# Performance work log

Hardware: AMD Instinct MI355X
Metric: run time of the kernel (lower is better)

Reference implementation:

```python
import jax, jax.numpy as jnp
import numpy as np

N_DATA = 542080   # N320 grid points
N_TRUNC = 40320   # O96 grid points
E_DOWN = 1084160
E_UP = 1084160
FEAT = 64


def setup_inputs() -> dict:
    key = jax.random.key(0)
    ks = jax.random.split(key, 7)
    x = jax.random.normal(ks[0], (2, 2, 1, N_DATA, FEAT), dtype=jnp.float32)
    down_src = jax.random.randint(ks[1], (E_DOWN,), 0, N_DATA)
    down_dst = jax.random.randint(ks[2], (E_DOWN,), 0, N_TRUNC)
    down_w = jax.random.uniform(ks[3], (E_DOWN,), dtype=jnp.float32)
    up_src = jax.random.randint(ks[4], (E_UP,), 0, N_TRUNC)
    up_dst = jax.random.randint(ks[5], (E_UP,), 0, N_DATA)
    up_w = jax.random.uniform(ks[6], (E_UP,), dtype=jnp.float32)
    return {"x": x, "down_src": down_src, "down_dst": down_dst, "down_w": down_w,
            "up_src": up_src, "up_dst": up_dst, "up_w": up_w}


def _sparse_project(h, src, dst, w, n_out):
    """Edge-weighted sparse projection: out[d] = sum_{e: dst[e]=d} w[e] * h[src[e]].

    h: (BE, n_in, F) -> (BE, n_out, F). Equivalent to left-multiplying by the
    sparse matrix A[dst, src] = w (summing duplicates), as SparseProjector does.
    """
    msgs = h[:, src, :] * w[None, :, None]            # (BE, E, F) gather + weight
    msgs = jnp.swapaxes(msgs, 0, 1)                   # (E, BE, F)
    out = jax.ops.segment_sum(msgs, dst, num_segments=n_out)  # (n_out, BE, F)
    return jnp.swapaxes(out, 0, 1)                    # (BE, n_out, F)


def reference(x, down_src, down_dst, down_w, up_src, up_dst, up_w):
    B, T, Ens, N, F = x.shape
    h = x[:, -1, ...]                                 # take last time step: (B, Ens, N, F)
    h = h.reshape(B * Ens, N, F)                      # (batch ensemble) grid features
    h = _sparse_project(h, down_src, down_dst, down_w, N_TRUNC)  # coarse grid
    h = _sparse_project(h, up_src, up_dst, up_w, N)              # back to full grid
    return h.reshape(B, Ens, N, F)
```

## Files before the change

### kernel.cpp

```cpp
#include <hip/hip_runtime.h>

#define FEAT 64
#define N_DATA 542080
#define N_TRUNC 40320
#define SCAN_TILE 4096


__global__ void histogram_dst(const int* __restrict__ dst, int n_edges,
                              int* __restrict__ counts) {
    int e = blockIdx.x * blockDim.x + threadIdx.x;
    if (e < n_edges) atomicAdd(&counts[dst[e]], 1);
}

__global__ void scan_block_sums(const int* __restrict__ counts, int n,
                                int* __restrict__ blockSums) {
    __shared__ int lds[256];
    int tid = threadIdx.x;
    int base = blockIdx.x * SCAN_TILE + tid * 16;
    int s = 0;
    #pragma unroll
    for (int i = 0; i < 16; ++i) {
        int idx = base + i;
        s += (idx < n) ? counts[idx] : 0;
    }
    lds[tid] = s;
    __syncthreads();
    for (int off = 128; off > 0; off >>= 1) {
        if (tid < off) lds[tid] += lds[tid + off];
        __syncthreads();
    }
    if (tid == 0) blockSums[blockIdx.x] = lds[0];
}

__global__ void scan_exclusive_blocksums(int* __restrict__ blockSums, int nblocks) {
    if (blockIdx.x == 0 && threadIdx.x == 0) {
        int acc = 0;
        for (int i = 0; i < nblocks; ++i) {
            int v = blockSums[i];
            blockSums[i] = acc;
            acc += v;
        }
    }
}

__global__ void scan_write_offsets(const int* __restrict__ counts, int n,
                                   const int* __restrict__ blockSums,
                                   int* __restrict__ offsets, int total_edges) {
    __shared__ int lds[256];
    int tid = threadIdx.x;
    int base = blockIdx.x * SCAN_TILE + tid * 16;
    int local[16];
    int s = 0;
    #pragma unroll
    for (int i = 0; i < 16; ++i) {
        int idx = base + i;
        int v = (idx < n) ? counts[idx] : 0;
        local[i] = s;
        s += v;
    }
    lds[tid] = s;
    __syncthreads();
    for (int off = 1; off < 256; off <<= 1) {
        int v = (tid >= off) ? lds[tid - off] : 0;
        __syncthreads();
        if (tid >= off) lds[tid] += v;
        __syncthreads();
    }
    int threadOffset = (tid == 0) ? 0 : lds[tid - 1];
    int blockOffset = blockSums[blockIdx.x];
    #pragma unroll
    for (int i = 0; i < 16; ++i) {
        int idx = base + i;
        if (idx < n) offsets[idx] = blockOffset + threadOffset + local[i];
    }
    if (blockIdx.x == 0 && tid == 0) offsets[n] = total_edges;
}

__global__ void build_csr(const int* __restrict__ src, const int* __restrict__ dst,
                          const float* __restrict__ w, int n_edges,
                          const int* __restrict__ offsets, int* __restrict__ cursor,
                          int2* __restrict__ csr_pair) {
    int e = blockIdx.x * blockDim.x + threadIdx.x;
    if (e >= n_edges) return;
    int d = dst[e];
    int pos = offsets[d] + atomicAdd(&cursor[d], 1);
    int2 p;
    p.x = src[e];
    p.y = __float_as_int(w[e]);
    csr_pair[pos] = p;
}

__global__ __launch_bounds__(256) void sparse_gather(
    const float* __restrict__ h, size_t h_bstride,
    float* __restrict__ out, size_t out_bstride,
    const int* __restrict__ offsets,
    const int2* __restrict__ csr_pair,
    int n_out)
{
    int id = blockIdx.x * blockDim.x + threadIdx.x;
    int d = id >> 4;
    int c = (id & 15) * 4;
    if (d >= n_out) return;

    int beg = offsets[d];
    int end = offsets[d + 1];

    float4 acc0 = make_float4(0.f, 0.f, 0.f, 0.f);
    float4 acc1 = make_float4(0.f, 0.f, 0.f, 0.f);

    for (int p = beg; p < end; ++p) {
        int2 pr = csr_pair[p];
        int   s  = pr.x;
        float ww = __int_as_float(pr.y);
        const float* row0 = h + (size_t)s * FEAT + c;
        const float* row1 = row0 + h_bstride;
        float4 v0 = *reinterpret_cast<const float4*>(row0);
        float4 v1 = *reinterpret_cast<const float4*>(row1);
        acc0.x += ww * v0.x; acc0.y += ww * v0.y;
        acc0.z += ww * v0.z; acc0.w += ww * v0.w;
        acc1.x += ww * v1.x; acc1.y += ww * v1.y;
        acc1.z += ww * v1.z; acc1.w += ww * v1.w;
    }
    float* o0 = out + (size_t)d * FEAT + c;
    *reinterpret_cast<float4*>(o0) = acc0;
    *reinterpret_cast<float4*>(o0 + out_bstride) = acc1;
}

__global__ __launch_bounds__(256) void sparse_project_atomic(
    const float* __restrict__ h, size_t h_bstride,
    float* __restrict__ out, size_t out_bstride,
    const int* __restrict__ src, const int* __restrict__ dst,
    const float* __restrict__ w, int n_edges)
{
    int id = blockIdx.x * blockDim.x + threadIdx.x;
    int e = id >> 4;
    int c = (id & 15) * 4;
    if (e >= n_edges) return;
    int b = blockIdx.y;
    const float* hb = h + (size_t)b * h_bstride;
    float*       ob = out + (size_t)b * out_bstride;
    int   s  = src[e];
    int   d  = dst[e];
    float ww = w[e];
    const float4 v = *reinterpret_cast<const float4*>(hb + (size_t)s * FEAT + c);
    float* op = ob + (size_t)d * FEAT + c;
    atomicAdd(op + 0, ww * v.x);
    atomicAdd(op + 1, ww * v.y);
    atomicAdd(op + 2, ww * v.z);
    atomicAdd(op + 3, ww * v.w);
}

static inline size_t align16(size_t v) { return (v + 15) & ~(size_t)15; }

extern "C" void kernel_launch(void* const* d_in, const int* in_sizes, int n_in,
                              void* d_out, int out_size, void* d_ws, size_t ws_size,
                              hipStream_t stream) {
    const float* x        = (const float*)d_in[0];
    const int*   down_src = (const int*)d_in[1];
    const int*   down_dst = (const int*)d_in[2];
    const float* down_w   = (const float*)d_in[3];
    const int*   up_src   = (const int*)d_in[4];
    const int*   up_dst   = (const int*)d_in[5];
    const float* up_w     = (const float*)d_in[6];
    float* out = (float*)d_out;

    const int e_down = in_sizes[1];
    const int e_up   = in_sizes[4];

    const float* x_last = x + (size_t)N_DATA * FEAT;
    const size_t x_bstride = (size_t)2 * N_DATA * FEAT;

    char* ws = (char*)d_ws;
    size_t off = 0;
    float* h_trunc   = (float*)(ws + off); off += align16((size_t)2 * N_TRUNC * FEAT * 4);
    int*   up_off    = (int*)(ws + off);   off += align16(((size_t)N_DATA + 1) * 4);
    int*   down_off  = (int*)(ws + off);   off += align16(((size_t)N_TRUNC + 1) * 4);
    int*   up_cur    = (int*)(ws + off);   off += align16((size_t)N_DATA * 4);
    int*   down_cur  = (int*)(ws + off);   off += align16((size_t)N_TRUNC * 4);
    int2*  up_csr    = (int2*)(ws + off);  off += align16((size_t)e_up * 8);
    int2*  down_csr  = (int2*)(ws + off);  off += align16((size_t)e_down * 8);
    int*   blockSums = (int*)(ws + off);   off += align16(1024);
    const size_t needed = off;

    if (ws_size < needed) {
        hipMemsetAsync(h_trunc, 0, (size_t)2 * N_TRUNC * FEAT * 4, stream);
        hipMemsetAsync(out, 0, (size_t)out_size * sizeof(float), stream);
        dim3 g1((e_down * 16 + 255) / 256, 2);
        sparse_project_atomic<<<g1, 256, 0, stream>>>(
            x_last, x_bstride, h_trunc, (size_t)N_TRUNC * FEAT,
            down_src, down_dst, down_w, e_down);
        dim3 g2((e_up * 16 + 255) / 256, 2);
        sparse_project_atomic<<<g2, 256, 0, stream>>>(
            h_trunc, (size_t)N_TRUNC * FEAT, out, (size_t)N_DATA * FEAT,
            up_src, up_dst, up_w, e_up);
        return;
    }

    const int nblk_down = (N_TRUNC + SCAN_TILE - 1) / SCAN_TILE;
    const int nblk_up   = (N_DATA  + SCAN_TILE - 1) / SCAN_TILE;

    hipMemsetAsync(down_cur, 0, (size_t)N_TRUNC * 4, stream);
    histogram_dst<<<(e_down + 255) / 256, 256, 0, stream>>>(down_dst, e_down, down_cur);
    scan_block_sums<<<nblk_down, 256, 0, stream>>>(down_cur, N_TRUNC, blockSums);
    scan_exclusive_blocksums<<<1, 64, 0, stream>>>(blockSums, nblk_down);
    scan_write_offsets<<<nblk_down, 256, 0, stream>>>(down_cur, N_TRUNC, blockSums, down_off, e_down);
    hipMemsetAsync(down_cur, 0, (size_t)N_TRUNC * 4, stream);
    build_csr<<<(e_down + 255) / 256, 256, 0, stream>>>(
        down_src, down_dst, down_w, e_down, down_off, down_cur, down_csr);

    hipMemsetAsync(up_cur, 0, (size_t)N_DATA * 4, stream);
    histogram_dst<<<(e_up + 255) / 256, 256, 0, stream>>>(up_dst, e_up, up_cur);
    scan_block_sums<<<nblk_up, 256, 0, stream>>>(up_cur, N_DATA, blockSums);
    scan_exclusive_blocksums<<<1, 64, 0, stream>>>(blockSums, nblk_up);
    scan_write_offsets<<<nblk_up, 256, 0, stream>>>(up_cur, N_DATA, blockSums, up_off, e_up);
    hipMemsetAsync(up_cur, 0, (size_t)N_DATA * 4, stream);
    build_csr<<<(e_up + 255) / 256, 256, 0, stream>>>(
        up_src, up_dst, up_w, e_up, up_off, up_cur, up_csr);

    {
        int threads = N_TRUNC * 16;
        sparse_gather<<<(threads + 255) / 256, 256, 0, stream>>>(
            x_last, x_bstride,
            h_trunc, (size_t)N_TRUNC * FEAT,
            down_off, down_csr, N_TRUNC);
    }
    {
        int threads = N_DATA * 16;
        sparse_gather<<<(threads + 255) / 256, 256, 0, stream>>>(
            h_trunc, (size_t)N_TRUNC * FEAT,
            out, (size_t)N_DATA * FEAT,
            up_off, up_csr, N_DATA);
    }
}
```

Baseline: 1.120 ms.

## Merge down/up CSR builds into one pass, unroll gather, use nontemporal output stores

The two CSR construction pipelines are merged into a single combined bucket space (down then up destinations), cutting the number of launches and memsets roughly in half. The serial block-sum scan is replaced with a parallel LDS scan, and count reset moves into the offset-writing kernel. The gather loop is unrolled by two to keep more loads in flight, and the final output uses nontemporal stores. The combined offsets rely on the up-pass offsets already including e_down, which matches the shared csr_all indexing.

```diff
diff --git a/kernel.cpp b/kernel.cpp
--- a/kernel.cpp
+++ b/kernel.cpp
@@ -3,13 +3,21 @@
 #define FEAT 64
 #define N_DATA 542080
 #define N_TRUNC 40320
+#define NB_TOTAL (N_TRUNC + N_DATA)
 #define SCAN_TILE 4096
 
-
-__global__ void histogram_dst(const int* __restrict__ dst, int n_edges,
-                              int* __restrict__ counts) {
+typedef float nfloat4 __attribute__((ext_vector_type(4)));
+
+
+__global__ void histogram_both(const int* __restrict__ ddst, int e_down,
+                               const int* __restrict__ udst, int e_up,
+                               int* __restrict__ counts) {
     int e = blockIdx.x * blockDim.x + threadIdx.x;
-    if (e < n_edges) atomicAdd(&counts[dst[e]], 1);
+    if (e < e_down) {
+        atomicAdd(&counts[ddst[e]], 1);
+    } else if (e < e_down + e_up) {
+        atomicAdd(&counts[N_TRUNC + udst[e - e_down]], 1);
+    }
 }
 
 __global__ void scan_block_sums(const int* __restrict__ counts, int n,
@@ -32,18 +40,21 @@
     if (tid == 0) blockSums[blockIdx.x] = lds[0];
 }
 
-__global__ void scan_exclusive_blocksums(int* __restrict__ blockSums, int nblocks) {
-    if (blockIdx.x == 0 && threadIdx.x == 0) {
-        int acc = 0;
-        for (int i = 0; i < nblocks; ++i) {
-            int v = blockSums[i];
-            blockSums[i] = acc;
-            acc += v;
-        }
-    }
-}
-
-__global__ void scan_write_offsets(const int* __restrict__ counts, int n,
+__global__ void scan_sums_block(int* __restrict__ blockSums, int nblocks) {
+    __shared__ int lds[256];
+    int tid = threadIdx.x;
+    lds[tid] = (tid < nblocks) ? blockSums[tid] : 0;
+    __syncthreads();
+    for (int off = 1; off < 256; off <<= 1) {
+        int v = (tid >= off) ? lds[tid - off] : 0;
+        __syncthreads();
+        if (tid >= off) lds[tid] += v;
+        __syncthreads();
+    }
+    if (tid < nblocks) blockSums[tid] = (tid == 0) ? 0 : lds[tid - 1];
+}
+
+__global__ void scan_write_offsets(int* __restrict__ counts, int n,
                                    const int* __restrict__ blockSums,
                                    int* __restrict__ offsets, int total_edges) {
     __shared__ int lds[256];
@@ -71,25 +82,38 @@
     #pragma unroll
     for (int i = 0; i < 16; ++i) {
         int idx = base + i;
-        if (idx < n) offsets[idx] = blockOffset + threadOffset + local[i];
+        if (idx < n) {
+            offsets[idx] = blockOffset + threadOffset + local[i];
+            counts[idx] = 0;
+        }
     }
     if (blockIdx.x == 0 && tid == 0) offsets[n] = total_edges;
 }
 
-__global__ void build_csr(const int* __restrict__ src, const int* __restrict__ dst,
-                          const float* __restrict__ w, int n_edges,
-                          const int* __restrict__ offsets, int* __restrict__ cursor,
-                          int2* __restrict__ csr_pair) {
+__global__ void build_csr_both(const int* __restrict__ dsrc, const int* __restrict__ ddst,
+                               const float* __restrict__ dw, int e_down,
+                               const int* __restrict__ usrc, const int* __restrict__ udst,
+                               const float* __restrict__ uw, int e_up,
+                               const int* __restrict__ offsets, int* __restrict__ cursor,
+                               int2* __restrict__ csr_pair) {
     int e = blockIdx.x * blockDim.x + threadIdx.x;
-    if (e >= n_edges) return;
-    int d = dst[e];
-    int pos = offsets[d] + atomicAdd(&cursor[d], 1);
+    int n = e_down + e_up;
+    if (e >= n) return;
+    int s, b; float wv;
+    if (e < e_down) {
+        s = dsrc[e]; b = ddst[e]; wv = dw[e];
+    } else {
+        int k = e - e_down;
+        s = usrc[k]; b = N_TRUNC + udst[k]; wv = uw[k];
+    }
+    int pos = offsets[b] + atomicAdd(&cursor[b], 1);
     int2 p;
-    p.x = src[e];
-    p.y = __float_as_int(w[e]);
+    p.x = s;
+    p.y = __float_as_int(wv);
     csr_pair[pos] = p;
 }
 
+template <bool NT>
 __global__ __launch_bounds__(256) void sparse_gather(
     const float* __restrict__ h, size_t h_bstride,
     float* __restrict__ out, size_t out_bstride,
@@ -108,22 +132,50 @@
     float4 acc0 = make_float4(0.f, 0.f, 0.f, 0.f);
     float4 acc1 = make_float4(0.f, 0.f, 0.f, 0.f);
 
-    for (int p = beg; p < end; ++p) {
+    const float* hc = h + c;
+    int p = beg;
+    for (; p + 2 <= end; p += 2) {
+        int2 pa = csr_pair[p];
+        int2 pb = csr_pair[p + 1];
+        float wa = __int_as_float(pa.y);
+        float wb = __int_as_float(pb.y);
+        const float* ra0 = hc + (size_t)pa.x * FEAT;
+        const float* rb0 = hc + (size_t)pb.x * FEAT;
+        float4 va0 = *reinterpret_cast<const float4*>(ra0);
+        float4 vb0 = *reinterpret_cast<const float4*>(rb0);
+        float4 va1 = *reinterpret_cast<const float4*>(ra0 + h_bstride);
+        float4 vb1 = *reinterpret_cast<const float4*>(rb0 + h_bstride);
+        acc0.x += wa * va0.x; acc0.y += wa * va0.y;
+        acc0.z += wa * va0.z; acc0.w += wa * va0.w;
+        acc1.x += wa * va1.x; acc1.y += wa * va1.y;
+        acc1.z += wa * va1.z; acc1.w += wa * va1.w;
+        acc0.x += wb * vb0.x; acc0.y += wb * vb0.y;
+        acc0.z += wb * vb0.z; acc0.w += wb * vb0.w;
+        acc1.x += wb * vb1.x; acc1.y += wb * vb1.y;
+        acc1.z += wb * vb1.z; acc1.w += wb * vb1.w;
+    }
+    if (p < end) {
         int2 pr = csr_pair[p];
-        int   s  = pr.x;
         float ww = __int_as_float(pr.y);
-        const float* row0 = h + (size_t)s * FEAT + c;
-        const float* row1 = row0 + h_bstride;
-        float4 v0 = *reinterpret_cast<const float4*>(row0);
-        float4 v1 = *reinterpret_cast<const float4*>(row1);
+        const float* r0 = hc + (size_t)pr.x * FEAT;
+        float4 v0 = *reinterpret_cast<const float4*>(r0);
+        float4 v1 = *reinterpret_cast<const float4*>(r0 + h_bstride);
         acc0.x += ww * v0.x; acc0.y += ww * v0.y;
         acc0.z += ww * v0.z; acc0.w += ww * v0.w;
         acc1.x += ww * v1.x; acc1.y += ww * v1.y;
         acc1.z += ww * v1.z; acc1.w += ww * v1.w;
     }
+
     float* o0 = out + (size_t)d * FEAT + c;
-    *reinterpret_cast<float4*>(o0) = acc0;
-    *reinterpret_cast<float4*>(o0 + out_bstride) = acc1;
+    if (NT) {
+        nfloat4 n0 = { acc0.x, acc0.y, acc0.z, acc0.w };
+        nfloat4 n1 = { acc1.x, acc1.y, acc1.z, acc1.w };
+        __builtin_nontemporal_store(n0, reinterpret_cast<nfloat4*>(o0));
+        __builtin_nontemporal_store(n1, reinterpret_cast<nfloat4*>(o0 + out_bstride));
+    } else {
+        *reinterpret_cast<float4*>(o0) = acc0;
+        *reinterpret_cast<float4*>(o0 + out_bstride) = acc1;
+    }
 }
 
 __global__ __launch_bounds__(256) void sparse_project_atomic(
@@ -164,8 +216,9 @@
     const float* up_w     = (const float*)d_in[6];
     float* out = (float*)d_out;
 
-    const int e_down = in_sizes[1];
-    const int e_up   = in_sizes[4];
+    const int e_down  = in_sizes[1];
+    const int e_up    = in_sizes[4];
+    const int e_total = e_down + e_up;
 
     const float* x_last = x + (size_t)N_DATA * FEAT;
     const size_t x_bstride = (size_t)2 * N_DATA * FEAT;
@@ -173,12 +226,9 @@
     char* ws = (char*)d_ws;
     size_t off = 0;
     float* h_trunc   = (float*)(ws + off); off += align16((size_t)2 * N_TRUNC * FEAT * 4);
-    int*   up_off    = (int*)(ws + off);   off += align16(((size_t)N_DATA + 1) * 4);
-    int*   down_off  = (int*)(ws + off);   off += align16(((size_t)N_TRUNC + 1) * 4);
-    int*   up_cur    = (int*)(ws + off);   off += align16((size_t)N_DATA * 4);
-    int*   down_cur  = (int*)(ws + off);   off += align16((size_t)N_TRUNC * 4);
-    int2*  up_csr    = (int2*)(ws + off);  off += align16((size_t)e_up * 8);
-    int2*  down_csr  = (int2*)(ws + off);  off += align16((size_t)e_down * 8);
+    int*   offsets   = (int*)(ws + off);   off += align16(((size_t)NB_TOTAL + 1) * 4);
+    int*   counts    = (int*)(ws + off);   off += align16((size_t)NB_TOTAL * 4);
+    int2*  csr_all   = (int2*)(ws + off);  off += align16((size_t)e_total * 8);
     int*   blockSums = (int*)(ws + off);   off += align16(1024);
     const size_t needed = off;
 
@@ -196,39 +246,31 @@
         return;
     }
 
-    const int nblk_down = (N_TRUNC + SCAN_TILE - 1) / SCAN_TILE;
-    const int nblk_up   = (N_DATA  + SCAN_TILE - 1) / SCAN_TILE;
-
-    hipMemsetAsync(down_cur, 0, (size_t)N_TRUNC * 4, stream);
-    histogram_dst<<<(e_down + 255) / 256, 256, 0, stream>>>(down_dst, e_down, down_cur);
-    scan_block_sums<<<nblk_down, 256, 0, stream>>>(down_cur, N_TRUNC, blockSums);
-    scan_exclusive_blocksums<<<1, 64, 0, stream>>>(blockSums, nblk_down);
-    scan_write_offsets<<<nblk_down, 256, 0, stream>>>(down_cur, N_TRUNC, blockSums, down_off, e_down);
-    hipMemsetAsync(down_cur, 0, (size_t)N_TRUNC * 4, stream);
-    build_csr<<<(e_down + 255) / 256, 256, 0, stream>>>(
-        down_src, down_dst, down_w, e_down, down_off, down_cur, down_csr);
-
-    hipMemsetAsync(up_cur, 0, (size_t)N_DATA * 4, stream);
-    histogram_dst<<<(e_up + 255) / 256, 256, 0, stream>>>(up_dst, e_up, up_cur);
-    scan_block_sums<<<nblk_up, 256, 0, stream>>>(up_cur, N_DATA, blockSums);
-    scan_exclusive_blocksums<<<1, 64, 0, stream>>>(blockSums, nblk_up);
-    scan_write_offsets<<<nblk_up, 256, 0, stream>>>(up_cur, N_DATA, blockSums, up_off, e_up);
-    hipMemsetAsync(up_cur, 0, (size_t)N_DATA * 4, stream);
-    build_csr<<<(e_up + 255) / 256, 256, 0, stream>>>(
-        up_src, up_dst, up_w, e_up, up_off, up_cur, up_csr);
+    const int nblk = (NB_TOTAL + SCAN_TILE - 1) / SCAN_TILE;
+
+    hipMemsetAsync(counts, 0, (size_t)NB_TOTAL * 4, stream);
+    histogram_both<<<(e_total + 255) / 256, 256, 0, stream>>>(
+        down_dst, e_down, up_dst, e_up, counts);
+    scan_block_sums<<<nblk, 256, 0, stream>>>(counts, NB_TOTAL, blockSums);
+    scan_sums_block<<<1, 256, 0, stream>>>(blockSums, nblk);
+    scan_write_offsets<<<nblk, 256, 0, stream>>>(counts, NB_TOTAL, blockSums, offsets, e_total);
+    build_csr_both<<<(e_total + 255) / 256, 256, 0, stream>>>(
+        down_src, down_dst, down_w, e_down,
+        up_src, up_dst, up_w, e_up,
+        offsets, counts, csr_all);
 
     {
         int threads = N_TRUNC * 16;
-        sparse_gather<<<(threads + 255) / 256, 256, 0, stream>>>(
+        sparse_gather<false><<<(threads + 255) / 256, 256, 0, stream>>>(
             x_last, x_bstride,
             h_trunc, (size_t)N_TRUNC * FEAT,
-            down_off, down_csr, N_TRUNC);
+            offsets, csr_all, N_TRUNC);
     }
     {
         int threads = N_DATA * 16;
-        sparse_gather<<<(threads + 255) / 256, 256, 0, stream>>>(
+        sparse_gather<true><<<(threads + 255) / 256, 256, 0, stream>>>(
             h_trunc, (size_t)N_TRUNC * FEAT,
             out, (size_t)N_DATA * FEAT,
-            up_off, up_csr, N_DATA);
-    }
-}
+            offsets + N_TRUNC, csr_all, N_DATA);
+    }
+}
```

Result: faster. 1.056 ms (-5.7%).
